# Performance work log

Hardware: AMD Instinct MI355X
Metric: run time of the kernel (lower is better)

Reference implementation:

```python
import jax, jax.numpy as jnp
import numpy as np


def _sliding_window_attention(q, k, v, window_size, padding_mask):
    # q,k,v: [B,H,S,D]; faithful to the torch code incl. clamped scatter_add
    # duplicates at boundaries and the (score==0 -> -inf) quirk.
    B, H, S, D = q.shape
    hw = window_size // 2
    kp = jnp.pad(k, ((0, 0), (0, 0), (hw, hw), (0, 0)))  # zero-pad seq dim
    # window gather positions into padded keys: [S, W+1]
    pos = jnp.arange(S)[:, None] + jnp.arange(window_size + 1)[None, :]
    kw = kp[:, :, pos, :]  # [B,H,S,W+1,D]
    scores = jnp.einsum('bhsd,bhswd->bhsw', q, kw) / jnp.sqrt(jnp.asarray(D, q.dtype))
    # scatter-add into full [B,H,S,S] with clamped column indices (duplicates sum)
    idx = jnp.clip(jnp.arange(S)[:, None] + jnp.arange(-hw, hw + 1)[None, :], 0, S - 1)  # [S,W+1]
    rows = jnp.arange(S)[:, None]
    full = jnp.zeros((B, H, S, S), q.dtype).at[:, :, rows, idx].add(scores)
    neg_inf = jnp.asarray(-jnp.inf, full.dtype)
    full = jnp.where(full == 0.0, neg_inf, full)
    if padding_mask is not None:
        pm = padding_mask[:, None, None, :]  # [B,1,1,S]
        full = jnp.where(pm == 0, neg_inf, full)
        full = jnp.where(jnp.swapaxes(pm, -1, -2) == 0, neg_inf, full)
    att = jax.nn.softmax(full, axis=-1)
    att = jnp.where(jnp.isnan(att), jnp.asarray(0.0, att.dtype), att)
    values = jnp.einsum('bhst,bhtd->bhsd', att, v)
    return values, att


def setup_inputs() -> dict:
    key = jax.random.key(0)
    ks = jax.random.split(key, 5)
    B, S, IN_DIM, E = 2, 2048, 512, 512
    x = jax.random.normal(ks[0], (B, S, IN_DIM), dtype=jnp.float32)
    padding_mask = jnp.ones((B, S), dtype=jnp.int32)
    qkv_w = jax.random.normal(ks[1], (3 * E, IN_DIM), dtype=jnp.float32) * 0.02
    qkv_b = jnp.zeros((3 * E,), dtype=jnp.float32)
    o_w = jax.random.normal(ks[2], (E, E), dtype=jnp.float32) * 0.02
    o_b = jnp.zeros((E,), dtype=jnp.float32)
    return {'x': x, 'padding_mask': padding_mask, 'qkv_w': qkv_w, 'qkv_b': qkv_b,
            'o_w': o_w, 'o_b': o_b, 'window_size': 256, 'num_heads': 8}


def reference(x, padding_mask, qkv_w, qkv_b, o_w, o_b, window_size, num_heads):
    B, S, _ = x.shape
    E3 = qkv_w.shape[0]
    E = E3 // 3
    head_dim = E // num_heads
    qkv = x @ qkv_w.T + qkv_b                         # [B,S,3E]
    qkv = qkv.reshape(B, S, num_heads, 3 * head_dim)
    qkv = jnp.transpose(qkv, (0, 2, 1, 3))            # [B,H,S,3*hd]
    q, k, v = jnp.split(qkv, 3, axis=-1)
    values, _ = _sliding_window_attention(q, k, v, window_size, padding_mask)
    values = jnp.transpose(values, (0, 2, 1, 3)).reshape(B, S, E)
    o = values @ o_w.T + o_b
    return o
```

## Files before the change

kernel.cpp:

```cpp
#include <hip/hip_runtime.h>
#include <hip/hip_bf16.h>
#include <math.h>


typedef __bf16 bf16x8 __attribute__((ext_vector_type(8)));
typedef float f32x4 __attribute__((ext_vector_type(4)));

__device__ __forceinline__ unsigned short f2bf(float f) {
  unsigned u = __float_as_uint(f);
  unsigned r = u + 0x7FFFu + ((u >> 16) & 1u);
  return (unsigned short)(r >> 16);
}

__device__ __forceinline__ void ldsdma16(void* lds, const void* g) {
  __builtin_amdgcn_global_load_lds(
      (const __attribute__((address_space(1))) unsigned int*)g,
      (__attribute__((address_space(3))) unsigned int*)lds, 16, 0, 0);
}

__global__ __launch_bounds__(256) void cvt3_kernel(
    const float* __restrict__ s0, unsigned short* __restrict__ d0, int n0,
    const float* __restrict__ s1, unsigned short* __restrict__ d1, int n1,
    const float* __restrict__ s2, unsigned short* __restrict__ d2, int n2) {
  int i4 = blockIdx.x * 256 + threadIdx.x;
  const int c0 = n0 >> 2, c1 = (n0 + n1) >> 2, c2 = (n0 + n1 + n2) >> 2;
  const float* s; unsigned short* d; int base4;
  if (i4 < c0)      { s = s0; d = d0; base4 = i4; }
  else if (i4 < c1) { s = s1; d = d1; base4 = i4 - c0; }
  else if (i4 < c2) { s = s2; d = d2; base4 = i4 - c1; }
  else return;
  float4 v = ((const float4*)s)[base4];
  ushort4 o;
  o.x = f2bf(v.x); o.y = f2bf(v.y); o.z = f2bf(v.z); o.w = f2bf(v.w);
  ((ushort4*)d)[base4] = o;
}

__global__ __launch_bounds__(256) void gemm_qkv(
    const __hip_bfloat16* __restrict__ A, const __hip_bfloat16* __restrict__ Bw,
    const float* __restrict__ bias,
    __hip_bfloat16* __restrict__ qp, __hip_bfloat16* __restrict__ kpb,
    unsigned short* __restrict__ vtb) {
  __shared__ __hip_bfloat16 As[128 * 32];
  __shared__ __hip_bfloat16 Bs[128 * 32];

  const int tid = threadIdx.x, wave = tid >> 6, lane = tid & 63;
  const int m0 = blockIdx.x * 128, n0 = blockIdx.y * 128;
  const int wm = (wave >> 1) * 64, wn = (wave & 1) * 64;
  const int cl = lane & 15, ko = (lane >> 4) * 8;
  const int srow = wave * 16 + (lane >> 2);
  const int scol = (lane & 3) * 8;

  f32x4 acc[4][4] = {};

  for (int k0 = 0; k0 < 512; k0 += 32) {
    __syncthreads();
    ldsdma16(&As[wave * 512],        A  + (size_t)(m0 + srow) * 512 + k0 + scol);
    ldsdma16(&As[2048 + wave * 512], A  + (size_t)(m0 + 64 + srow) * 512 + k0 + scol);
    ldsdma16(&Bs[wave * 512],        Bw + (size_t)(n0 + srow) * 512 + k0 + scol);
    ldsdma16(&Bs[2048 + wave * 512], Bw + (size_t)(n0 + 64 + srow) * 512 + k0 + scol);
    __syncthreads();

    bf16x8 af[4], bf[4];
#pragma unroll
    for (int i = 0; i < 4; i++)
      af[i] = *(const bf16x8*)(&As[(wm + cl + i * 16) * 32 + ko]);
#pragma unroll
    for (int i = 0; i < 4; i++)
      bf[i] = *(const bf16x8*)(&Bs[(wn + cl + i * 16) * 32 + ko]);
#pragma unroll
    for (int mi = 0; mi < 4; mi++)
#pragma unroll
      for (int ni = 0; ni < 4; ni++)
        acc[mi][ni] = __builtin_amdgcn_mfma_f32_16x16x32_bf16(
            af[mi], bf[ni], acc[mi][ni], 0, 0, 0);
  }

  const int crow = (lane >> 4) * 4;
#pragma unroll
  for (int mi = 0; mi < 4; mi++) {
    const int mb = m0 + wm + mi * 16 + crow;
    const int bq = mb >> 11, sl = mb & 2047;
#pragma unroll
    for (int ni = 0; ni < 4; ni++) {
      const int n = n0 + wn + ni * 16 + cl;
      const int h = n / 192;
      const int rem = n - h * 192;
      const int cat = rem >> 6;
      const int d = rem & 63;
      const float bv = bias[n];
      const size_t bh = (size_t)bq * 8 + h;
      if (cat == 2) {
        ushort4 o;
        o.x = f2bf(acc[mi][ni][0] + bv);
        o.y = f2bf(acc[mi][ni][1] + bv);
        o.z = f2bf(acc[mi][ni][2] + bv);
        o.w = f2bf(acc[mi][ni][3] + bv);
        *(ushort4*)(vtb + bh * 131072 + (sl >> 3) * 512 + d * 8 + (sl & 7)) = o;
      } else {
        __hip_bfloat16* dst = (cat == 0) ? qp : kpb;
        const float sc = (cat == 0) ? 0.18033688011112042f : 1.0f;
#pragma unroll
        for (int r = 0; r < 4; r++)
          dst[(bh * 2048 + sl + r) * 64 + d] =
              __float2bfloat16((acc[mi][ni][r] + bv) * sc);
      }
    }
  }
}

__global__ __launch_bounds__(256) void attn_mfma(
    const __hip_bfloat16* __restrict__ qp, const __hip_bfloat16* __restrict__ kp,
    const __hip_bfloat16* __restrict__ vt, const int* __restrict__ pm,
    __hip_bfloat16* __restrict__ vals) {
  __shared__ __hip_bfloat16 sKP[320 * 72];
  __shared__ float sCM[320];

  const int tid = threadIdx.x, wave = tid >> 6, lane = tid & 63;
  const int bid = blockIdx.x;
  const int s0 = (bid & 31) * 64;
  const int bh = bid >> 5;
  const int b = bh >> 3, h = bh & 7;
  const int t0 = s0 - 128;
  const int cl = lane & 15;
  const int g4 = (lane >> 4) * 4;
  const int ko = (lane >> 4) * 8;

  {
    const int e = (tid & 7) * 8;
#pragma unroll
    for (int i = 0; i < 10; i++) {
      int row = (tid >> 3) + i * 32;
      int t = t0 + row; t = min(max(t, 0), 2047);
      *(uint4*)(&sKP[row * 72 + e]) =
          *(const uint4*)(kp + ((size_t)bh * 2048 + t) * 64 + e);
    }
  }
  for (int c = tid; c < 320; c += 256) {
    int t = t0 + c;
    bool ok = (t >= 0 && t < 2048) && (pm[b * 2048 + t] != 0);
    sCM[c] = ok ? 0.0f : -3.0e38f;
  }
  __syncthreads();

  const __hip_bfloat16* qrow =
      qp + ((size_t)bh * 2048 + s0 + wave * 16 + cl) * 64 + ko;
  bf16x8 aq0 = *(const bf16x8*)(qrow);
  bf16x8 aq1 = *(const bf16x8*)(qrow + 32);

  f32x4 acc[17];
#pragma unroll
  for (int i = 0; i < 17; i++) {
    const int krow = (wave + i) * 16 + cl;
    bf16x8 b0 = *(const bf16x8*)(&sKP[krow * 72 + ko]);
    bf16x8 b1 = *(const bf16x8*)(&sKP[krow * 72 + ko + 32]);
    f32x4 z = {};
    z = __builtin_amdgcn_mfma_f32_16x16x32_bf16(aq0, b0, z, 0, 0, 0);
    acc[i] = __builtin_amdgcn_mfma_f32_16x16x32_bf16(aq1, b1, z, 0, 0, 0);
  }

  float mrow[4] = {-3.0e38f, -3.0e38f, -3.0e38f, -3.0e38f};
#pragma unroll
  for (int i = 0; i < 17; i++) {
    const float ca = sCM[(wave + i) * 16 + cl];
#pragma unroll
    for (int r = 0; r < 4; r++) {
      float sv = acc[i][r] + ca;
      if (i == 0) {
        if (cl < g4 + r) sv = -3.0e38f;
      } else if (i == 16) {
        if (cl > g4 + r) sv = -3.0e38f;
      }
      acc[i][r] = sv;
      mrow[r] = fmaxf(mrow[r], sv);
    }
  }
#pragma unroll
  for (int r = 0; r < 4; r++)
#pragma unroll
    for (int off = 1; off < 16; off <<= 1)
      mrow[r] = fmaxf(mrow[r], __shfl_xor(mrow[r], off));

  float lsum[4] = {0.f, 0.f, 0.f, 0.f};
#pragma unroll
  for (int i = 0; i < 17; i++)
#pragma unroll
    for (int r = 0; r < 4; r++) {
      float p = exp2f(acc[i][r] - mrow[r]);
      acc[i][r] = p;
      lsum[r] += p;
    }
#pragma unroll
  for (int r = 0; r < 4; r++)
#pragma unroll
    for (int off = 1; off < 16; off <<= 1)
      lsum[r] += __shfl_xor(lsum[r], off);

  __syncthreads();

  __hip_bfloat16* sp = sKP + wave * 5248;
#pragma unroll
  for (int i = 0; i < 17; i++) {
    const int c = (wave + i) * 16 + cl;
#pragma unroll
    for (int r = 0; r < 4; r++)
      sp[(g4 + r) * 328 + c] = __float2bfloat16(acc[i][r]);
  }
  {
    const int zt = (wave & 1) ? (wave - 1) : (wave + 17);
    const int zc = zt * 16 + cl;
#pragma unroll
    for (int r = 0; r < 4; r++)
      sp[(g4 + r) * 328 + zc] = __float2bfloat16(0.f);
  }

  f32x4 oacc[4] = {};
  const int k0 = wave >> 1;
  const __hip_bfloat16* vbase = vt + (size_t)bh * 131072;
#pragma unroll
  for (int ks = 0; ks < 9; ks++) {
    const int kk = (k0 + ks) * 32 + ko;
    bf16x8 pa = *(const bf16x8*)(&sp[cl * 328 + kk]);
    int tv = t0 + kk; tv = min(max(tv, 0), 2040);
    const __hip_bfloat16* vrow = vbase + (tv >> 3) * 512;
#pragma unroll
    for (int ni = 0; ni < 4; ni++) {
      const int d = ni * 16 + cl;
      bf16x8 vb = *(const bf16x8*)(vrow + d * 8);
      oacc[ni] = __builtin_amdgcn_mfma_f32_16x16x32_bf16(pa, vb, oacc[ni], 0, 0, 0);
    }
  }

#pragma unroll
  for (int r = 0; r < 4; r++) {
    float linv = 1.0f / fmaxf(lsum[r], 1e-20f);
    const int qr = wave * 16 + g4 + r;
    if (sCM[qr + 128] != 0.0f) linv = 0.0f;
    const size_t obase = ((size_t)(b * 2048 + s0 + qr)) * 512 + h * 64 + cl;
#pragma unroll
    for (int ni = 0; ni < 4; ni++)
      vals[obase + ni * 16] = __float2bfloat16(oacc[ni][r] * linv);
  }
}

__global__ __launch_bounds__(256) void gemm_out(
    const __hip_bfloat16* __restrict__ A, const __hip_bfloat16* __restrict__ Bw,
    const float* __restrict__ bias, float* __restrict__ C) {
  __shared__ __hip_bfloat16 As[64 * 32];
  __shared__ __hip_bfloat16 Bs[128 * 32];

  const int tid = threadIdx.x, wave = tid >> 6, lane = tid & 63;
  const int m0 = blockIdx.x * 64, n0 = blockIdx.y * 128;
  const int wm = (wave >> 1) * 32, wn = (wave & 1) * 64;
  const int cl = lane & 15, ko = (lane >> 4) * 8;
  const int srow = wave * 16 + (lane >> 2);
  const int scol = (lane & 3) * 8;

  f32x4 acc[2][4] = {};

  for (int k0 = 0; k0 < 512; k0 += 32) {
    __syncthreads();
    ldsdma16(&As[wave * 512],        A  + (size_t)(m0 + srow) * 512 + k0 + scol);
    ldsdma16(&Bs[wave * 512],        Bw + (size_t)(n0 + srow) * 512 + k0 + scol);
    ldsdma16(&Bs[2048 + wave * 512], Bw + (size_t)(n0 + 64 + srow) * 512 + k0 + scol);
    __syncthreads();

    bf16x8 af[2], bf[4];
#pragma unroll
    for (int i = 0; i < 2; i++)
      af[i] = *(const bf16x8*)(&As[(wm + cl + i * 16) * 32 + ko]);
#pragma unroll
    for (int i = 0; i < 4; i++)
      bf[i] = *(const bf16x8*)(&Bs[(wn + cl + i * 16) * 32 + ko]);
#pragma unroll
    for (int mi = 0; mi < 2; mi++)
#pragma unroll
      for (int ni = 0; ni < 4; ni++)
        acc[mi][ni] = __builtin_amdgcn_mfma_f32_16x16x32_bf16(
            af[mi], bf[ni], acc[mi][ni], 0, 0, 0);
  }

  const int crow = (lane >> 4) * 4;
#pragma unroll
  for (int mi = 0; mi < 2; mi++) {
#pragma unroll
    for (int ni = 0; ni < 4; ni++) {
      const int n = n0 + wn + ni * 16 + cl;
      const float bv = bias[n];
      const int mb = m0 + wm + mi * 16 + crow;
#pragma unroll
      for (int r = 0; r < 4; r++)
        C[(size_t)(mb + r) * 512 + n] = acc[mi][ni][r] + bv;
    }
  }
}

extern "C" void kernel_launch(void* const* d_in, const int* in_sizes, int n_in,
                              void* d_out, int out_size, void* d_ws, size_t ws_size,
                              hipStream_t stream) {
  const float* x     = (const float*)d_in[0];
  const int*   pm    = (const int*)d_in[1];
  const float* qkv_w = (const float*)d_in[2];
  const float* qkv_b = (const float*)d_in[3];
  const float* o_w   = (const float*)d_in[4];
  const float* o_b   = (const float*)d_in[5];
  float* out = (float*)d_out;

  __hip_bfloat16* wsb   = (__hip_bfloat16*)d_ws;
  __hip_bfloat16* xb    = wsb;
  __hip_bfloat16* wqkvb = wsb + 2097152;
  __hip_bfloat16* wob   = wsb + 2883584;
  __hip_bfloat16* qp    = wsb + 3145728;
  __hip_bfloat16* kp    = wsb + 5242880;
  __hip_bfloat16* vt    = wsb + 7340032;
  __hip_bfloat16* vals  = wsb + 9437184;

  dim3 blk(256);
  cvt3_kernel<<<dim3(3072), blk, 0, stream>>>(
      x, (unsigned short*)xb, 2097152,
      qkv_w, (unsigned short*)wqkvb, 786432,
      o_w, (unsigned short*)wob, 262144);
  gemm_qkv<<<dim3(32, 12), blk, 0, stream>>>(
      xb, wqkvb, qkv_b, qp, kp, (unsigned short*)vt);
  attn_mfma<<<dim3(512), blk, 0, stream>>>(qp, kp, vt, pm, vals);
  gemm_out<<<dim3(64, 4), blk, 0, stream>>>(vals, wob, o_b, out);
}
```

Measured before the change: 115.4 us.

## Split each attention row tile across two waves with shared-memory softmax reduction

The attention kernel now runs 512 threads per block, and each 16-row query tile is handled by a pair of waves that split the 17 key tiles (9/8) and the 9 PV k-steps (5/4). Row max and row sum are exchanged through small shared arrays, and the odd wave's partial output is added into the even wave's result through LDS before the write. The aim is more waves in flight and fewer registers per wave on the MI355X. The cost is extra __syncthreads barriers and LDS traffic for the partial reductions.

```diff
diff --git a/kernel.cpp b/kernel.cpp
--- a/kernel.cpp
+++ b/kernel.cpp
@@ -108,14 +108,17 @@
   }
 }
 
-__global__ __launch_bounds__(256) void attn_mfma(
+__global__ __launch_bounds__(512) void attn_mfma(
     const __hip_bfloat16* __restrict__ qp, const __hip_bfloat16* __restrict__ kp,
     const __hip_bfloat16* __restrict__ vt, const int* __restrict__ pm,
     __hip_bfloat16* __restrict__ vals) {
   __shared__ __hip_bfloat16 sKP[320 * 72];
   __shared__ float sCM[320];
+  __shared__ float sMrow[4][2][16];
+  __shared__ float sLsum[4][2][16];
 
   const int tid = threadIdx.x, wave = tid >> 6, lane = tid & 63;
+  const int pair = wave >> 1, parity = wave & 1;
   const int bid = blockIdx.x;
   const int s0 = (bid & 31) * 64;
   const int bh = bid >> 5;
@@ -128,14 +131,14 @@
   {
     const int e = (tid & 7) * 8;
 #pragma unroll
-    for (int i = 0; i < 10; i++) {
-      int row = (tid >> 3) + i * 32;
+    for (int i = 0; i < 5; i++) {
+      int row = (tid >> 3) + i * 64;
       int t = t0 + row; t = min(max(t, 0), 2047);
       *(uint4*)(&sKP[row * 72 + e]) =
           *(const uint4*)(kp + ((size_t)bh * 2048 + t) * 64 + e);
     }
   }
-  for (int c = tid; c < 320; c += 256) {
+  for (int c = tid; c < 320; c += 512) {
     int t = t0 + c;
     bool ok = (t >= 0 && t < 2048) && (pm[b * 2048 + t] != 0);
     sCM[c] = ok ? 0.0f : -3.0e38f;
@@ -143,35 +146,41 @@
   __syncthreads();
 
   const __hip_bfloat16* qrow =
-      qp + ((size_t)bh * 2048 + s0 + wave * 16 + cl) * 64 + ko;
+      qp + ((size_t)bh * 2048 + s0 + pair * 16 + cl) * 64 + ko;
   bf16x8 aq0 = *(const bf16x8*)(qrow);
   bf16x8 aq1 = *(const bf16x8*)(qrow + 32);
 
-  f32x4 acc[17];
-#pragma unroll
-  for (int i = 0; i < 17; i++) {
-    const int krow = (wave + i) * 16 + cl;
-    bf16x8 b0 = *(const bf16x8*)(&sKP[krow * 72 + ko]);
-    bf16x8 b1 = *(const bf16x8*)(&sKP[krow * 72 + ko + 32]);
-    f32x4 z = {};
-    z = __builtin_amdgcn_mfma_f32_16x16x32_bf16(aq0, b0, z, 0, 0, 0);
-    acc[i] = __builtin_amdgcn_mfma_f32_16x16x32_bf16(aq1, b1, z, 0, 0, 0);
+  const int nt = 9 - parity;
+  const int tbase = pair + parity * 9;
+  f32x4 acc[9] = {};
+#pragma unroll
+  for (int j = 0; j < 9; j++) {
+    if (j < nt) {
+      const int krow = (tbase + j) * 16 + cl;
+      bf16x8 b0 = *(const bf16x8*)(&sKP[krow * 72 + ko]);
+      bf16x8 b1 = *(const bf16x8*)(&sKP[krow * 72 + ko + 32]);
+      f32x4 z = {};
+      z = __builtin_amdgcn_mfma_f32_16x16x32_bf16(aq0, b0, z, 0, 0, 0);
+      acc[j] = __builtin_amdgcn_mfma_f32_16x16x32_bf16(aq1, b1, z, 0, 0, 0);
+    }
   }
 
   float mrow[4] = {-3.0e38f, -3.0e38f, -3.0e38f, -3.0e38f};
 #pragma unroll
-  for (int i = 0; i < 17; i++) {
-    const float ca = sCM[(wave + i) * 16 + cl];
-#pragma unroll
-    for (int r = 0; r < 4; r++) {
-      float sv = acc[i][r] + ca;
-      if (i == 0) {
-        if (cl < g4 + r) sv = -3.0e38f;
-      } else if (i == 16) {
-        if (cl > g4 + r) sv = -3.0e38f;
-      }
-      acc[i][r] = sv;
-      mrow[r] = fmaxf(mrow[r], sv);
+  for (int j = 0; j < 9; j++) {
+    if (j < nt) {
+      const float ca = sCM[(tbase + j) * 16 + cl];
+#pragma unroll
+      for (int r = 0; r < 4; r++) {
+        float sv = acc[j][r] + ca;
+        if (parity == 0 && j == 0) {
+          if (cl < g4 + r) sv = -3.0e38f;
+        } else if (parity == 1 && j == 7) {
+          if (cl > g4 + r) sv = -3.0e38f;
+        }
+        acc[j][r] = sv;
+        mrow[r] = fmaxf(mrow[r], sv);
+      }
     }
   }
 #pragma unroll
@@ -179,66 +188,103 @@
 #pragma unroll
     for (int off = 1; off < 16; off <<= 1)
       mrow[r] = fmaxf(mrow[r], __shfl_xor(mrow[r], off));
+  if (cl == 0) {
+#pragma unroll
+    for (int r = 0; r < 4; r++) sMrow[pair][parity][g4 + r] = mrow[r];
+  }
+  __syncthreads();
+
+  float mr[4];
+#pragma unroll
+  for (int r = 0; r < 4; r++)
+    mr[r] = fmaxf(sMrow[pair][0][g4 + r], sMrow[pair][1][g4 + r]);
 
   float lsum[4] = {0.f, 0.f, 0.f, 0.f};
 #pragma unroll
-  for (int i = 0; i < 17; i++)
-#pragma unroll
-    for (int r = 0; r < 4; r++) {
-      float p = exp2f(acc[i][r] - mrow[r]);
-      acc[i][r] = p;
-      lsum[r] += p;
-    }
+  for (int j = 0; j < 9; j++) {
+    if (j < nt) {
+#pragma unroll
+      for (int r = 0; r < 4; r++) {
+        float pv = exp2f(acc[j][r] - mr[r]);
+        acc[j][r] = pv;
+        lsum[r] += pv;
+      }
+    }
+  }
 #pragma unroll
   for (int r = 0; r < 4; r++)
 #pragma unroll
     for (int off = 1; off < 16; off <<= 1)
       lsum[r] += __shfl_xor(lsum[r], off);
-
-  __syncthreads();
-
-  __hip_bfloat16* sp = sKP + wave * 5248;
-#pragma unroll
-  for (int i = 0; i < 17; i++) {
-    const int c = (wave + i) * 16 + cl;
-#pragma unroll
-    for (int r = 0; r < 4; r++)
-      sp[(g4 + r) * 328 + c] = __float2bfloat16(acc[i][r]);
-  }
-  {
-    const int zt = (wave & 1) ? (wave - 1) : (wave + 17);
+  if (cl == 0) {
+#pragma unroll
+    for (int r = 0; r < 4; r++) sLsum[pair][parity][g4 + r] = lsum[r];
+  }
+
+  __hip_bfloat16* sp = sKP + pair * 5248;
+#pragma unroll
+  for (int j = 0; j < 9; j++) {
+    if (j < nt) {
+      const int c = (tbase + j) * 16 + cl;
+#pragma unroll
+      for (int r = 0; r < 4; r++)
+        sp[(g4 + r) * 328 + c] = __float2bfloat16(acc[j][r]);
+    }
+  }
+  if (parity == 1) {
+    const int zt = (pair & 1) ? (pair - 1) : (pair + 17);
     const int zc = zt * 16 + cl;
 #pragma unroll
     for (int r = 0; r < 4; r++)
       sp[(g4 + r) * 328 + zc] = __float2bfloat16(0.f);
   }
+  __syncthreads();
 
   f32x4 oacc[4] = {};
-  const int k0 = wave >> 1;
+  const int k0p = pair >> 1;
+  const int klo = parity ? 5 : 0, khi = parity ? 9 : 5;
   const __hip_bfloat16* vbase = vt + (size_t)bh * 131072;
 #pragma unroll
   for (int ks = 0; ks < 9; ks++) {
-    const int kk = (k0 + ks) * 32 + ko;
-    bf16x8 pa = *(const bf16x8*)(&sp[cl * 328 + kk]);
-    int tv = t0 + kk; tv = min(max(tv, 0), 2040);
-    const __hip_bfloat16* vrow = vbase + (tv >> 3) * 512;
-#pragma unroll
-    for (int ni = 0; ni < 4; ni++) {
-      const int d = ni * 16 + cl;
-      bf16x8 vb = *(const bf16x8*)(vrow + d * 8);
-      oacc[ni] = __builtin_amdgcn_mfma_f32_16x16x32_bf16(pa, vb, oacc[ni], 0, 0, 0);
-    }
-  }
-
-#pragma unroll
-  for (int r = 0; r < 4; r++) {
-    float linv = 1.0f / fmaxf(lsum[r], 1e-20f);
-    const int qr = wave * 16 + g4 + r;
-    if (sCM[qr + 128] != 0.0f) linv = 0.0f;
-    const size_t obase = ((size_t)(b * 2048 + s0 + qr)) * 512 + h * 64 + cl;
-#pragma unroll
-    for (int ni = 0; ni < 4; ni++)
-      vals[obase + ni * 16] = __float2bfloat16(oacc[ni][r] * linv);
+    if (ks >= klo && ks < khi) {
+      const int kk = (k0p + ks) * 32 + ko;
+      bf16x8 pa = *(const bf16x8*)(&sp[cl * 328 + kk]);
+      int tv = t0 + kk; tv = min(max(tv, 0), 2040);
+      const __hip_bfloat16* vrow = vbase + (tv >> 3) * 512;
+#pragma unroll
+      for (int ni = 0; ni < 4; ni++) {
+        const int d = ni * 16 + cl;
+        bf16x8 vb = *(const bf16x8*)(vrow + d * 8);
+        oacc[ni] = __builtin_amdgcn_mfma_f32_16x16x32_bf16(pa, vb, oacc[ni], 0, 0, 0);
+      }
+    }
+  }
+  __syncthreads();
+
+  float* sO = (float*)sKP;
+  if (parity == 1) {
+#pragma unroll
+    for (int r = 0; r < 4; r++)
+#pragma unroll
+      for (int ni = 0; ni < 4; ni++)
+        sO[pair * 1040 + (g4 + r) * 65 + ni * 16 + cl] = oacc[ni][r];
+  }
+  __syncthreads();
+
+  if (parity == 0) {
+#pragma unroll
+    for (int r = 0; r < 4; r++) {
+      const float lt = lsum[r] + sLsum[pair][1][g4 + r];
+      float linv = 1.0f / fmaxf(lt, 1e-20f);
+      const int qr = pair * 16 + g4 + r;
+      if (sCM[qr + 128] != 0.0f) linv = 0.0f;
+      const size_t obase = ((size_t)(b * 2048 + s0 + qr)) * 512 + h * 64 + cl;
+#pragma unroll
+      for (int ni = 0; ni < 4; ni++) {
+        float o = oacc[ni][r] + sO[pair * 1040 + (g4 + r) * 65 + ni * 16 + cl];
+        vals[obase + ni * 16] = __float2bfloat16(o * linv);
+      }
+    }
   }
 }
 
@@ -321,6 +367,6 @@
       o_w, (unsigned short*)wob, 262144);
   gemm_qkv<<<dim3(32, 12), blk, 0, stream>>>(
       xb, wqkvb, qkv_b, qp, kp, (unsigned short*)vt);
-  attn_mfma<<<dim3(512), blk, 0, stream>>>(qp, kp, vt, pm, vals);
+  attn_mfma<<<dim3(512), dim3(512), 0, stream>>>(qp, kp, vt, pm, vals);
   gemm_out<<<dim3(64, 4), blk, 0, stream>>>(vals, wob, o_b, out);
 }
```

Result: no change. 116.0 us (+0.6%).
